# Kernel optimization log

Measured on AMD Instinct MI355X. Metric: run time of the kernel, lower is better.

Reference implementation:

```python
import jax, jax.numpy as jnp
import numpy as np

B, C, F = 4, 3, 5
HO, WO = 256, 256
HI, WI = HO + F - 1, WO + F - 1


def setup_inputs() -> dict:
    key = jax.random.key(0)
    k = jax.random.split(key, 6)
    return {
        "tensorInput": jax.random.normal(k[0], (B, C, HI, WI), dtype=jnp.float32),
        "tensorVertical": jax.random.uniform(k[1], (B, F, HO, WO), dtype=jnp.float32),
        "tensorHorizontal": jax.random.uniform(k[2], (B, F, HO, WO), dtype=jnp.float32),
        "tensorOffsetX": jax.random.normal(k[3], (B, F * F, HO, WO), dtype=jnp.float32),
        "tensorOffsetY": jax.random.normal(k[4], (B, F * F, HO, WO), dtype=jnp.float32),
        "tensorMask": jax.random.uniform(k[5], (B, F * F, HO, WO), dtype=jnp.float32),
    }


def _dsepconv(inp, vertical, horizontal, offset_x, offset_y, mask):
    b, c, hin, win = inp.shape
    f = vertical.shape[1]
    ho, wo = vertical.shape[2], vertical.shape[3]
    half = (f - 1) / 2.0

    fy = jnp.arange(f, dtype=inp.dtype).reshape(f, 1, 1, 1)
    fx = jnp.arange(f, dtype=inp.dtype).reshape(1, f, 1, 1)
    hg = jnp.arange(ho, dtype=inp.dtype).reshape(1, 1, ho, 1)
    wg = jnp.arange(wo, dtype=inp.dtype).reshape(1, 1, 1, wo)

    off_y = offset_y.reshape(b, f, f, ho, wo)  # note: code uses offset_y for delta_x
    off_x = offset_x.reshape(b, f, f, ho, wo)  # and offset_x for delta_y

    # sample positions per tap, [B,F,F,Ho,Wo]
    px = jnp.clip(off_y + wg + fx - half + 1.0, 0.0, win - 1)
    py = jnp.clip(off_x + hg + fy - half + 1.0, 0.0, hin - 1)

    left_f = jnp.floor(px)
    top_f = jnp.floor(py)
    wx = 1.0 - (px - left_f)  # bilinear weights
    wy = 1.0 - (py - top_f)

    l = left_f.astype(jnp.int32)
    t = top_f.astype(jnp.int32)
    r = jnp.minimum(l + 1, win - 1)
    btm = jnp.minimum(t + 1, hin - 1)

    def gather(img, yi, xi):
        return img[:, yi, xi]

    g = jax.vmap(gather)
    v_tl = g(inp, t, l)
    v_tr = g(inp, t, r)
    v_bl = g(inp, btm, l)
    v_br = g(inp, btm, r)

    wx_ = wx[:, None]  # add channel axis -> [B,1,F,F,Ho,Wo]
    wy_ = wy[:, None]
    val = (v_tl * wx_ * wy_ + v_tr * (1 - wx_) * wy_
           + v_bl * wx_ * (1 - wy_) + v_br * (1 - wx_) * (1 - wy_))

    # separable filter x mask per tap: [B,F,F,Ho,Wo]
    w_tap = vertical[:, :, None] * horizontal[:, None, :] * mask.reshape(b, f, f, ho, wo)
    # accumulate over the F*F taps
    return jnp.sum(val * w_tap[:, None], axis=(2, 3))  # [B,C,Ho,Wo]


def reference(tensorInput, tensorVertical, tensorHorizontal, tensorOffsetX, tensorOffsetY, tensorMask):
    return _dsepconv(tensorInput, tensorVertical, tensorHorizontal,
                     tensorOffsetX, tensorOffsetY, tensorMask)
```

## Files before the change

kernel.cpp:

```cpp
#include <hip/hip_runtime.h>
#include <hip/hip_fp16.h>

constexpr int B  = 4;
constexpr int C  = 3;
constexpr int F  = 5;
constexpr int HO = 256;
constexpr int WO = 256;
constexpr int HI = HO + F - 1;
constexpr int WI = WO + F - 1;
constexpr int P  = HO * WO;
constexpr int FF = F * F;
constexpr int PI = HI * WI;

constexpr int TROWS = 21;
constexpr int TCOLS = 80;
constexpr int TSTRIDE = 81;
constexpr int TN = TROWS * TCOLS;
constexpr int AMAX = (TROWS - 2) * TSTRIDE + (TCOLS - 2);

__device__ __forceinline__ uint2 pack3(float a, float b, float c) {
    __half2 ab = __floats2half2_rn(a, b);
    __half2 cz = __floats2half2_rn(c, 0.0f);
    uint2 r;
    r.x = *reinterpret_cast<const unsigned int*>(&ab);
    r.y = *reinterpret_cast<const unsigned int*>(&cz);
    return r;
}

__device__ __forceinline__ void fmacc(uint2 v, float w,
                                      float& a0, float& a1, float& a2) {
    __half2 ab = *reinterpret_cast<const __half2*>(&v.x);
    __half2 cz = *reinterpret_cast<const __half2*>(&v.y);
    a0 += __half2float(__low2half(ab))  * w;
    a1 += __half2float(__high2half(ab)) * w;
    a2 += __half2float(__low2half(cz))  * w;
}

__global__ __launch_bounds__(256, 4) void dsepconv_kernel(
    const float* __restrict__ inp,
    const float* __restrict__ vert,
    const float* __restrict__ horz,
    const float* __restrict__ offX,
    const float* __restrict__ offY,
    const float* __restrict__ mask,
    float* __restrict__ out)
{
    __shared__ uint2 tileq[TROWS * TSTRIDE];

    const int tid  = threadIdx.x;
    const int lane = tid & 63;
    const int wave = tid >> 6;

    const int bx   = blockIdx.x;
    const int x0   = (bx & 3) * 64;
    const int y0   = ((bx >> 2) & 63) * 4;
    const int b    = bx >> 8;

    const float* in0 = inp + (size_t)b * C * PI;
    const float* in1 = in0 + PI;
    const float* in2 = in1 + PI;

    const int ry0 = y0 - 7;
    const int cx0 = x0 - 7;
#pragma unroll 1
    for (int e = tid; e < TN; e += 256) {
        int trow = e / TCOLS;
        int tcol = e - trow * TCOLS;
        int gy = min(max(ry0 + trow, 0), HI - 1);
        int gx = min(max(cx0 + tcol, 0), WI - 1);
        int g = gy * WI + gx;
        tileq[trow * TSTRIDE + tcol] = pack3(in0[g], in1[g], in2[g]);
    }
    __syncthreads();

    const int x   = x0 + lane;
    const int y   = y0 + wave;
    const int pix = y * WO + x;

    const float* offXb = offX + (size_t)b * FF * P + pix;
    const float* offYb = offY + (size_t)b * FF * P + pix;
    const float* maskb = mask + (size_t)b * FF * P + pix;
    const float* vb    = vert + (size_t)b * F * P + pix;
    const float* hb    = horz + (size_t)b * F * P + pix;

    float acc0 = 0.f, acc1 = 0.f, acc2 = 0.f;

#pragma unroll 1
    for (int i = 0; i < F; ++i) {
        const float v = vb[i * P];
        const float py_base = (float)(y + i - 1);

#pragma unroll 1
        for (int j = 0; j < F; ++j) {
            const int k = i * F + j;

            float oy = offYb[k * P];
            float ox = offXb[k * P];
            float m  = maskb[k * P];
            float h  = hb[j * P];

            float px = fminf(fmaxf(oy + (float)(x + j - 1), 0.0f), (float)(WI - 1));
            float py = fminf(fmaxf(ox + py_base, 0.0f), (float)(HI - 1));

            float lf = floorf(px);
            float tf = floorf(py);
            int l = (int)lf;
            int t = (int)tf;
            float wx = 1.0f - (px - lf);
            float wy = 1.0f - (py - tf);

            float w   = v * h * m;
            float wyw = wy * w;
            float wbw = w - wyw;
            float wtl = wx * wyw;
            float wtr = wyw - wtl;
            float wbl = wx * wbw;
            float wbr = wbw - wbl;

            int lt = t - ry0;
            int ll = l - cx0;
            bool ok = ((unsigned)lt <= TROWS - 2) & ((unsigned)ll <= TCOLS - 2);

            int a = min(max(lt * TSTRIDE + ll, 0), AMAX);

            uint2 g_tl = tileq[a];
            uint2 g_tr = tileq[a + 1];
            uint2 g_bl = tileq[a + TSTRIDE];
            uint2 g_br = tileq[a + TSTRIDE + 1];

            if (__any(!ok)) {
                if (!ok) {
                    int r  = min(l + 1, WI - 1);
                    int bt = min(t + 1, HI - 1);
                    int o_tl = t * WI + l,  o_tr = t * WI + r;
                    int o_bl = bt * WI + l, o_br = bt * WI + r;
                    g_tl = pack3(in0[o_tl], in1[o_tl], in2[o_tl]);
                    g_tr = pack3(in0[o_tr], in1[o_tr], in2[o_tr]);
                    g_bl = pack3(in0[o_bl], in1[o_bl], in2[o_bl]);
                    g_br = pack3(in0[o_br], in1[o_br], in2[o_br]);
                }
            }

            fmacc(g_tl, wtl, acc0, acc1, acc2);
            fmacc(g_tr, wtr, acc0, acc1, acc2);
            fmacc(g_bl, wbl, acc0, acc1, acc2);
            fmacc(g_br, wbr, acc0, acc1, acc2);
        }
    }

    float* ob = out + (size_t)b * C * P + pix;
    ob[0]     = acc0;
    ob[P]     = acc1;
    ob[2 * P] = acc2;
}

extern "C" void kernel_launch(void* const* d_in, const int* in_sizes, int n_in,
                              void* d_out, int out_size, void* d_ws, size_t ws_size,
                              hipStream_t stream) {
    const float* inp  = (const float*)d_in[0];
    const float* vert = (const float*)d_in[1];
    const float* horz = (const float*)d_in[2];
    const float* offX = (const float*)d_in[3];
    const float* offY = (const float*)d_in[4];
    const float* mask = (const float*)d_in[5];
    float* out = (float*)d_out;

    dim3 block(256);
    dim3 grid(B * (HO / 4) * (WO / 64));
    dsepconv_kernel<<<grid, block, 0, stream>>>(inp, vert, horz, offX, offY, mask, out);
}
```

Baseline: 28.85 us.

## Split filter taps across two waves per pixel row with shared-memory reduction

Doubles the block to 512 threads and has each pair of waves share one output row, one wave handling taps 0-11 and the other 12-24. The partial sums are combined through a small shared-memory buffer. This halves the serial tap loop per thread and adds more waves to hide the latency of global offset/mask loads. The costs are an extra barrier, extra shared memory, redundant vertical-filter loads (no longer hoisted per row), and an uneven 12/13 tap split.

Result: faster. 26.54 us (-8.0%).

```diff
diff --git a/kernel.cpp b/kernel.cpp
--- a/kernel.cpp
+++ b/kernel.cpp
@@ -36,7 +36,7 @@
     a2 += __half2float(__low2half(cz))  * w;
 }
 
-__global__ __launch_bounds__(256, 4) void dsepconv_kernel(
+__global__ __launch_bounds__(512, 8) void dsepconv_kernel(
     const float* __restrict__ inp,
     const float* __restrict__ vert,
     const float* __restrict__ horz,
@@ -46,10 +46,13 @@
     float* __restrict__ out)
 {
     __shared__ uint2 tileq[TROWS * TSTRIDE];
+    __shared__ float red[4][3][64];
 
     const int tid  = threadIdx.x;
     const int lane = tid & 63;
     const int wave = tid >> 6;
+    const int wrow = wave >> 1;
+    const int half = wave & 1;
 
     const int bx   = blockIdx.x;
     const int x0   = (bx & 3) * 64;
@@ -63,7 +66,7 @@
     const int ry0 = y0 - 7;
     const int cx0 = x0 - 7;
 #pragma unroll 1
-    for (int e = tid; e < TN; e += 256) {
+    for (int e = tid; e < TN; e += 512) {
         int trow = e / TCOLS;
         int tcol = e - trow * TCOLS;
         int gy = min(max(ry0 + trow, 0), HI - 1);
@@ -74,7 +77,7 @@
     __syncthreads();
 
     const int x   = x0 + lane;
-    const int y   = y0 + wave;
+    const int y   = y0 + wrow;
     const int pix = y * WO + x;
 
     const float* offXb = offX + (size_t)b * FF * P + pix;
@@ -85,73 +88,81 @@
 
     float acc0 = 0.f, acc1 = 0.f, acc2 = 0.f;
 
-#pragma unroll 1
-    for (int i = 0; i < F; ++i) {
-        const float v = vb[i * P];
-        const float py_base = (float)(y + i - 1);
+    const int k0 = half ? 12 : 0;
+    const int k1 = half ? 25 : 12;
 
 #pragma unroll 1
-        for (int j = 0; j < F; ++j) {
-            const int k = i * F + j;
+    for (int k = k0; k < k1; ++k) {
+        const int i = k / F;
+        const int j = k - i * F;
 
-            float oy = offYb[k * P];
-            float ox = offXb[k * P];
-            float m  = maskb[k * P];
-            float h  = hb[j * P];
+        float oy = offYb[k * P];
+        float ox = offXb[k * P];
+        float m  = maskb[k * P];
+        float h  = hb[j * P];
+        float v  = vb[i * P];
 
-            float px = fminf(fmaxf(oy + (float)(x + j - 1), 0.0f), (float)(WI - 1));
-            float py = fminf(fmaxf(ox + py_base, 0.0f), (float)(HI - 1));
+        float px = fminf(fmaxf(oy + (float)(x + j - 1), 0.0f), (float)(WI - 1));
+        float py = fminf(fmaxf(ox + (float)(y + i - 1), 0.0f), (float)(HI - 1));
 
-            float lf = floorf(px);
-            float tf = floorf(py);
-            int l = (int)lf;
-            int t = (int)tf;
-            float wx = 1.0f - (px - lf);
-            float wy = 1.0f - (py - tf);
+        float lf = floorf(px);
+        float tf = floorf(py);
+        int l = (int)lf;
+        int t = (int)tf;
+        float wx = 1.0f - (px - lf);
+        float wy = 1.0f - (py - tf);
 
-            float w   = v * h * m;
-            float wyw = wy * w;
-            float wbw = w - wyw;
-            float wtl = wx * wyw;
-            float wtr = wyw - wtl;
-            float wbl = wx * wbw;
-            float wbr = wbw - wbl;
+        float w   = v * h * m;
+        float wyw = wy * w;
+        float wbw = w - wyw;
+        float wtl = wx * wyw;
+        float wtr = wyw - wtl;
+        float wbl = wx * wbw;
+        float wbr = wbw - wbl;
 
-            int lt = t - ry0;
-            int ll = l - cx0;
-            bool ok = ((unsigned)lt <= TROWS - 2) & ((unsigned)ll <= TCOLS - 2);
+        int lt = t - ry0;
+        int ll = l - cx0;
+        bool ok = ((unsigned)lt <= TROWS - 2) & ((unsigned)ll <= TCOLS - 2);
 
-            int a = min(max(lt * TSTRIDE + ll, 0), AMAX);
+        int a = min(max(lt * TSTRIDE + ll, 0), AMAX);
 
-            uint2 g_tl = tileq[a];
-            uint2 g_tr = tileq[a + 1];
-            uint2 g_bl = tileq[a + TSTRIDE];
-            uint2 g_br = tileq[a + TSTRIDE + 1];
+        uint2 g_tl = tileq[a];
+        uint2 g_tr = tileq[a + 1];
+        uint2 g_bl = tileq[a + TSTRIDE];
+        uint2 g_br = tileq[a + TSTRIDE + 1];
 
-            if (__any(!ok)) {
-                if (!ok) {
-                    int r  = min(l + 1, WI - 1);
-                    int bt = min(t + 1, HI - 1);
-                    int o_tl = t * WI + l,  o_tr = t * WI + r;
-                    int o_bl = bt * WI + l, o_br = bt * WI + r;
-                    g_tl = pack3(in0[o_tl], in1[o_tl], in2[o_tl]);
-                    g_tr = pack3(in0[o_tr], in1[o_tr], in2[o_tr]);
-                    g_bl = pack3(in0[o_bl], in1[o_bl], in2[o_bl]);
-                    g_br = pack3(in0[o_br], in1[o_br], in2[o_br]);
-                }
+        if (__any(!ok)) {
+            if (!ok) {
+                int r  = min(l + 1, WI - 1);
+                int bt = min(t + 1, HI - 1);
+                int o_tl = t * WI + l,  o_tr = t * WI + r;
+                int o_bl = bt * WI + l, o_br = bt * WI + r;
+                g_tl = pack3(in0[o_tl], in1[o_tl], in2[o_tl]);
+                g_tr = pack3(in0[o_tr], in1[o_tr], in2[o_tr]);
+                g_bl = pack3(in0[o_bl], in1[o_bl], in2[o_bl]);
+                g_br = pack3(in0[o_br], in1[o_br], in2[o_br]);
             }
+        }
 
-            fmacc(g_tl, wtl, acc0, acc1, acc2);
-            fmacc(g_tr, wtr, acc0, acc1, acc2);
-            fmacc(g_bl, wbl, acc0, acc1, acc2);
-            fmacc(g_br, wbr, acc0, acc1, acc2);
-        }
+        fmacc(g_tl, wtl, acc0, acc1, acc2);
+        fmacc(g_tr, wtr, acc0, acc1, acc2);
+        fmacc(g_bl, wbl, acc0, acc1, acc2);
+        fmacc(g_br, wbr, acc0, acc1, acc2);
     }
 
-    float* ob = out + (size_t)b * C * P + pix;
-    ob[0]     = acc0;
-    ob[P]     = acc1;
-    ob[2 * P] = acc2;
+    if (half) {
+        red[wrow][0][lane] = acc0;
+        red[wrow][1][lane] = acc1;
+        red[wrow][2][lane] = acc2;
+    }
+    __syncthreads();
+
+    if (!half) {
+        float* ob = out + (size_t)b * C * P + pix;
+        ob[0]     = acc0 + red[wrow][0][lane];
+        ob[P]     = acc1 + red[wrow][1][lane];
+        ob[2 * P] = acc2 + red[wrow][2][lane];
+    }
 }
 
 extern "C" void kernel_launch(void* const* d_in, const int* in_sizes, int n_in,
@@ -165,7 +176,7 @@
     const float* mask = (const float*)d_in[5];
     float* out = (float*)d_out;
 
-    dim3 block(256);
+    dim3 block(512);
     dim3 grid(B * (HO / 4) * (WO / 64));
     dsepconv_kernel<<<grid, block, 0, stream>>>(inp, vert, horz, offX, offY, mask, out);
 }
```
